# Optimization experiments

Measured on AMD Instinct MI355X. Metric: run time of the kernel, lower is better.

The kernel has to match this reference:

```python
import jax, jax.numpy as jnp
import numpy as np
import math

EMBED_DIM = 1024
NUM_HEADS = 16
HEAD_DIM = EMBED_DIM // NUM_HEADS


def setup_inputs() -> dict:
    key = jax.random.key(0)
    ks = jax.random.split(key, 12)
    B, N = 2, 2048
    s = 1.0 / math.sqrt(EMBED_DIM)
    inp = {
        "query": jax.random.normal(ks[0], (B, N, EMBED_DIM), jnp.float32),
        "key": jax.random.normal(ks[1], (B, N, EMBED_DIM), jnp.float32),
        "value": jax.random.normal(ks[2], (B, N, EMBED_DIM), jnp.float32),
        "Wq": jax.random.normal(ks[3], (EMBED_DIM, EMBED_DIM), jnp.float32) * s,
        "bq": jnp.zeros((EMBED_DIM,), jnp.float32),
        "Wk": jax.random.normal(ks[4], (EMBED_DIM, EMBED_DIM), jnp.float32) * s,
        "bk": jnp.zeros((EMBED_DIM,), jnp.float32),
        "Wv": jax.random.normal(ks[5], (EMBED_DIM, EMBED_DIM), jnp.float32) * s,
        "bv": jnp.zeros((EMBED_DIM,), jnp.float32),
        "Wo": jax.random.normal(ks[6], (EMBED_DIM, EMBED_DIM), jnp.float32) * s,
        "bo": jnp.zeros((EMBED_DIM,), jnp.float32),
        "gate": jnp.zeros((NUM_HEADS,), jnp.float32),
    }
    return inp


def reference(query, key, value, Wq, bq, Wk, bk, Wv, bv, Wo, bo, gate):
    B, Nq, _ = query.shape
    Nk = key.shape[1]
    H, D = NUM_HEADS, HEAD_DIM
    # projections (Linear: x @ W.T + b); split heads -> [B, H, N, D]
    q = (query @ Wq.T + bq).reshape(B, Nq, H, D).transpose(0, 2, 1, 3)
    k = (key @ Wk.T + bk).reshape(B, Nk, H, D).transpose(0, 2, 1, 3)
    v = (value @ Wv.T + bv).reshape(B, Nk, H, D).transpose(0, 2, 1, 3)
    # scaled logits with per-head sigmoid gate folded into the scale
    scale = jax.nn.sigmoid(gate) / math.sqrt(D)  # [H]
    logits = jnp.einsum("bhqd,bhkd->bhqk", q, k) * scale[None, :, None, None]
    attn = jax.nn.softmax(logits, axis=-1)
    out = jnp.einsum("bhqk,bhkd->bhqd", attn, v)
    out = out.transpose(0, 2, 1, 3).reshape(B, Nq, H * D)
    return out @ Wo.T + bo
```

## Files before the change

kernel.cpp:

```cpp
#include <hip/hip_runtime.h>
#include <hip/hip_bf16.h>
#include <cstdint>


#define DEV __device__ __forceinline__
typedef __attribute__((ext_vector_type(8))) short bf16x8;
typedef __attribute__((ext_vector_type(4))) float f32x4;
typedef unsigned short u16;

DEV void async16(const void* g, void* l) {
  __builtin_amdgcn_global_load_lds(
      (const __attribute__((address_space(1))) unsigned int*)g,
      (__attribute__((address_space(3))) unsigned int*)l, 16, 0, 0);
}

DEV u16 bf16_rne(float f) {
  unsigned int u = __builtin_bit_cast(unsigned int, f);
  u += 0x7FFFu + ((u >> 16) & 1u);
  return (u16)(u >> 16);
}

DEV u16 cvt16(float x) {
  __hip_bfloat16 h = __float2bfloat16(x);
  return __builtin_bit_cast(u16, h);
}

DEV unsigned pack2(float lo, float hi) {
  return (unsigned)cvt16(lo) | ((unsigned)cvt16(hi) << 16);
}

__global__ __launch_bounds__(256) void cast_all(
    const float* __restrict__ q, const float* __restrict__ k, const float* __restrict__ v,
    const float* __restrict__ Wq, const float* __restrict__ Wk,
    const float* __restrict__ Wv, const float* __restrict__ Wo,
    u16* __restrict__ XQ, u16* __restrict__ XK, u16* __restrict__ XV,
    u16* __restrict__ WQB, u16* __restrict__ WKB, u16* __restrict__ WVB,
    u16* __restrict__ WOB) {
  int idx = blockIdx.x * 256 + threadIdx.x;
  const float* src; u16* dst; int i;
  if      (idx <  524288) { src = q;  dst = XQ;  i = idx; }
  else if (idx < 1048576) { src = k;  dst = XK;  i = idx -  524288; }
  else if (idx < 1572864) { src = v;  dst = XV;  i = idx - 1048576; }
  else if (idx < 1703936) { src = Wq; dst = WQB; i = idx - 1572864; }
  else if (idx < 1835008) { src = Wk; dst = WKB; i = idx - 1703936; }
  else if (idx < 1966080) { src = Wv; dst = WVB; i = idx - 1835008; }
  else                    { src = Wo; dst = WOB; i = idx - 1966080; }
  const float4* p = (const float4*)src + (size_t)i * 2;
  float4 a = p[0], b = p[1];
  union { u16 us[8]; uint4 vv; } u;
  u.us[0] = bf16_rne(a.x); u.us[1] = bf16_rne(a.y);
  u.us[2] = bf16_rne(a.z); u.us[3] = bf16_rne(a.w);
  u.us[4] = bf16_rne(b.x); u.us[5] = bf16_rne(b.y);
  u.us[6] = bf16_rne(b.z); u.us[7] = bf16_rne(b.w);
  ((uint4*)dst)[i] = u.vv;
}

__global__ __launch_bounds__(256, 3) void gemm_qkv(
    const u16* __restrict__ XQ, const u16* __restrict__ XK, const u16* __restrict__ XV,
    const u16* __restrict__ Wb,
    const float* __restrict__ bq, const float* __restrict__ bkb, const float* __restrict__ bv,
    const float* __restrict__ gate,
    u16* __restrict__ QB, u16* __restrict__ KB, u16* __restrict__ VTB) {
  __shared__ __attribute__((aligned(16))) u16 As[2][128 * 32];
  __shared__ __attribute__((aligned(16))) u16 Bs[2][128 * 32];
  const int t = threadIdx.x, lane = t & 63, w = t >> 6;
  const int l15 = lane & 15, quad = lane >> 4;
  const int seg = blockIdx.x >> 8, inner = blockIdx.x & 255;
  const int bm = inner >> 3, bn = inner & 7;
  const int m0 = bm << 7, n0 = bn << 7;
  const u16* A = (seg == 0) ? XQ : (seg == 1) ? XK : XV;
  const u16* W = Wb + (long)seg * 1048576;
  const int wm = (w >> 1) << 6, wn = (w & 1) << 6;
  const int r0 = t >> 2, cc0 = (t & 3) * 8;
  const u16* gA0 = A + (long)(m0 + r0) * 1024 + cc0;
  const u16* gA1 = gA0 + 64 * 1024;
  const u16* gB0 = W + (long)(n0 + r0) * 1024 + cc0;
  const u16* gB1 = gB0 + 64 * 1024;

  async16(gA0, &As[0][t * 8]); async16(gA1, &As[0][(t + 256) * 8]);
  async16(gB0, &Bs[0][t * 8]); async16(gB1, &Bs[0][(t + 256) * 8]);

  f32x4 acc[4][4] = {};
  for (int k0 = 0; k0 < 1024; k0 += 32) {
    const int cur = (k0 >> 5) & 1;
    __syncthreads();
    if (k0 + 32 < 1024) {
      const int kn = k0 + 32, nb = cur ^ 1;
      async16(gA0 + kn, &As[nb][t * 8]); async16(gA1 + kn, &As[nb][(t + 256) * 8]);
      async16(gB0 + kn, &Bs[nb][t * 8]); async16(gB1 + kn, &Bs[nb][(t + 256) * 8]);
    }
    bf16x8 af[4], bfm[4];
#pragma unroll
    for (int i = 0; i < 4; i++)
      af[i] = *(const bf16x8*)&As[cur][(wm + i * 16 + l15) * 32 + quad * 8];
#pragma unroll
    for (int j = 0; j < 4; j++)
      bfm[j] = *(const bf16x8*)&Bs[cur][(wn + j * 16 + l15) * 32 + quad * 8];
#pragma unroll
    for (int i = 0; i < 4; i++)
#pragma unroll
      for (int j = 0; j < 4; j++)
        acc[i][j] = __builtin_amdgcn_mfma_f32_16x16x32_bf16(af[i], bfm[j], acc[i][j], 0, 0, 0);
  }

  if (seg == 2) {
#pragma unroll
    for (int i = 0; i < 4; i++) {
      int token = m0 + wm + i * 16 + quad * 4;
      int bb_ = token >> 11, n = token & 2047;
#pragma unroll
      for (int j = 0; j < 4; j++) {
        int col = n0 + wn + j * 16 + l15;
        float bb = bv[col];
        union { u16 us[4]; uint2 u2; } pk;
#pragma unroll
        for (int r = 0; r < 4; r++) pk.us[r] = bf16_rne(acc[i][j][r] + bb);
        *(uint2*)&VTB[(long)(bb_ * 1024 + col) * 2048 + n] = pk.u2;
      }
    }
  } else {
    const float* bias = seg ? bkb : bq;
    u16* C = seg ? KB : QB;
#pragma unroll
    for (int j = 0; j < 4; j++) {
      int col = n0 + wn + j * 16 + l15;
      float bb = bias[col];
      float scl = 1.f;
      if (seg == 0) {
        float g = gate[col >> 6];
        float sig = 1.f / (1.f + __builtin_amdgcn_exp2f(-g * 1.44269504f));
        scl = sig * 0.125f * 1.44269504f;
      }
#pragma unroll
      for (int i = 0; i < 4; i++) {
        int row = m0 + wm + i * 16 + quad * 4;
#pragma unroll
        for (int r = 0; r < 4; r++)
          C[(long)(row + r) * 1024 + col] = bf16_rne((acc[i][j][r] + bb) * scl);
      }
    }
  }
}

__global__ __launch_bounds__(256, 2) void gemm_out(
    const u16* __restrict__ A, const u16* __restrict__ W,
    const float* __restrict__ bias, float* __restrict__ Cf) {
  __shared__ __attribute__((aligned(16))) u16 As[2][64 * 32];
  __shared__ __attribute__((aligned(16))) u16 Bs[2][128 * 32];
  const int t = threadIdx.x, lane = t & 63, w = t >> 6;
  const int l15 = lane & 15, quad = lane >> 4;
  const int bm = blockIdx.x >> 3, bn = blockIdx.x & 7;
  const int m0 = bm << 6, n0 = bn << 7;
  const int wm = (w >> 1) << 5, wn = (w & 1) << 6;
  const int r0 = t >> 2, cc0 = (t & 3) * 8;
  const u16* gA = A + (long)(m0 + r0) * 1024 + cc0;
  const u16* gB0 = W + (long)(n0 + r0) * 1024 + cc0;
  const u16* gB1 = gB0 + 64 * 1024;

  async16(gA, &As[0][t * 8]);
  async16(gB0, &Bs[0][t * 8]); async16(gB1, &Bs[0][(t + 256) * 8]);

  f32x4 acc[2][4] = {};
  for (int k0 = 0; k0 < 1024; k0 += 32) {
    const int cur = (k0 >> 5) & 1;
    __syncthreads();
    if (k0 + 32 < 1024) {
      const int kn = k0 + 32, nb = cur ^ 1;
      async16(gA + kn, &As[nb][t * 8]);
      async16(gB0 + kn, &Bs[nb][t * 8]); async16(gB1 + kn, &Bs[nb][(t + 256) * 8]);
    }
    bf16x8 af[2], bfm[4];
#pragma unroll
    for (int i = 0; i < 2; i++)
      af[i] = *(const bf16x8*)&As[cur][(wm + i * 16 + l15) * 32 + quad * 8];
#pragma unroll
    for (int j = 0; j < 4; j++)
      bfm[j] = *(const bf16x8*)&Bs[cur][(wn + j * 16 + l15) * 32 + quad * 8];
#pragma unroll
    for (int i = 0; i < 2; i++)
#pragma unroll
      for (int j = 0; j < 4; j++)
        acc[i][j] = __builtin_amdgcn_mfma_f32_16x16x32_bf16(af[i], bfm[j], acc[i][j], 0, 0, 0);
  }

#pragma unroll
  for (int j = 0; j < 4; j++) {
    int col = n0 + wn + j * 16 + l15;
    float bb = bias[col];
#pragma unroll
    for (int i = 0; i < 2; i++) {
      int row = m0 + wm + i * 16 + quad * 4;
#pragma unroll
      for (int r = 0; r < 4; r++)
        Cf[(long)(row + r) * 1024 + col] = acc[i][j][r] + bb;
    }
  }
}

__global__ __launch_bounds__(128, 4) void attn_kernel(
    const u16* __restrict__ Q, const u16* __restrict__ Kb,
    const u16* __restrict__ Vt, u16* __restrict__ Op, float* __restrict__ lp) {
  __shared__ __attribute__((aligned(16))) u16 Ks[2][32 * 64];
  __shared__ __attribute__((aligned(16))) u16 Vs[2][64 * 32];
  __shared__ __attribute__((aligned(16))) u16 Ps[2][32 * 32];
  const int t = threadIdx.x, lane = t & 63, w = t >> 6;
  const int l15 = lane & 15, quad = lane >> 4;
  const int qt = blockIdx.x >> 1, ksp = blockIdx.x & 1;
  const int h = blockIdx.y, b = blockIdx.z;
  const int q0 = qt * 64, tok0 = b * 2048, key0 = ksp * 1024;
  const u16* Kbase = Kb + (long)tok0 * 1024 + h * 64;
  const u16* Vbase = Vt + (long)(b * 1024 + h * 64) * 2048;

  bf16x8 aq[2][2];
#pragma unroll
  for (int i = 0; i < 2; i++) {
    long row = tok0 + q0 + w * 32 + i * 16 + l15;
#pragma unroll
    for (int ks = 0; ks < 2; ks++)
      aq[i][ks] = *(const bf16x8*)&Q[row * 1024 + h * 64 + ks * 32 + quad * 8];
  }

#pragma unroll
  for (int i = 0; i < 2; i++) {
    int c = i * 128 + t;
    int rk = c >> 3, ck = c & 7, cks = ck ^ ((rk >> 1) & 7);
    async16(&Kbase[(long)(key0 + rk) * 1024 + cks * 8], &Ks[0][c * 8]);
    int rv = c >> 2, cv = c & 3, cvs = cv ^ ((rv >> 1) & 3);
    async16(&Vbase[(long)rv * 2048 + key0 + cvs * 8], &Vs[0][c * 8]);
  }

  float l_st[2][4] = {};
  f32x4 O[2][4] = {};

  for (int kt = 0; kt < 32; kt++) {
    const int cur = kt & 1;
    __syncthreads();
    if (kt + 1 < 32) {
      const int k0n = key0 + (kt + 1) * 32, nb = cur ^ 1;
#pragma unroll
      for (int i = 0; i < 2; i++) {
        int c = i * 128 + t;
        int rk = c >> 3, ck = c & 7, cks = ck ^ ((rk >> 1) & 7);
        async16(&Kbase[(long)(k0n + rk) * 1024 + cks * 8], &Ks[nb][c * 8]);
        int rv = c >> 2, cv = c & 3, cvs = cv ^ ((rv >> 1) & 3);
        async16(&Vbase[(long)rv * 2048 + k0n + cvs * 8], &Vs[nb][c * 8]);
      }
    }

    f32x4 s[2][2] = {};
#pragma unroll
    for (int ks = 0; ks < 2; ks++) {
      bf16x8 bk_[2];
#pragma unroll
      for (int j = 0; j < 2; j++) {
        int rl = 2 * l15 + j;
        bk_[j] = *(const bf16x8*)&Ks[cur][rl * 64 + (((ks * 4 + quad) ^ (l15 & 7))) * 8];
      }
#pragma unroll
      for (int i = 0; i < 2; i++)
#pragma unroll
        for (int j = 0; j < 2; j++)
          s[i][j] = __builtin_amdgcn_mfma_f32_16x16x32_bf16(aq[i][ks], bk_[j], s[i][j], 0, 0, 0);
    }

#pragma unroll
    for (int i = 0; i < 2; i++) {
#pragma unroll
      for (int r = 0; r < 4; r++) {
        float p0 = __builtin_amdgcn_exp2f(s[i][0][r]);
        float p1 = __builtin_amdgcn_exp2f(s[i][1][r]);
        l_st[i][r] += p0 + p1;
        const int prow = i * 16 + quad * 4 + r;
        const int chs = (l15 >> 2) ^ ((prow >> 1) & 3);
        *(unsigned*)&Ps[w][prow * 32 + chs * 8 + (l15 & 3) * 2] = pack2(p0, p1);
      }
    }

    {
      bf16x8 ap[2], bv_[4];
#pragma unroll
      for (int i = 0; i < 2; i++) {
        int rl = i * 16 + l15;
        ap[i] = *(const bf16x8*)&Ps[w][rl * 32 + ((quad ^ ((rl >> 1) & 3))) * 8];
      }
#pragma unroll
      for (int dj = 0; dj < 4; dj++) {
        int rl = dj * 16 + l15;
        bv_[dj] = *(const bf16x8*)&Vs[cur][rl * 32 + ((quad ^ ((rl >> 1) & 3))) * 8];
      }
#pragma unroll
      for (int i = 0; i < 2; i++)
#pragma unroll
        for (int dj = 0; dj < 4; dj++)
          O[i][dj] = __builtin_amdgcn_mfma_f32_16x16x32_bf16(ap[i], bv_[dj], O[i][dj], 0, 0, 0);
    }
  }

#pragma unroll
  for (int i = 0; i < 2; i++) {
#pragma unroll
    for (int r = 0; r < 4; r++) {
      float ls = l_st[i][r];
      ls += __shfl_xor(ls, 1); ls += __shfl_xor(ls, 2);
      ls += __shfl_xor(ls, 4); ls += __shfl_xor(ls, 8);
      long row = tok0 + q0 + w * 32 + i * 16 + quad * 4 + r;
#pragma unroll
      for (int dj = 0; dj < 4; dj++)
        Op[(long)ksp * 4194304 + row * 1024 + h * 64 + dj * 16 + l15] = cvt16(O[i][dj][r]);
      if (l15 == 0) lp[ksp * 65536 + (int)row * 16 + h] = ls;
    }
  }
}

__global__ __launch_bounds__(256) void merge_kernel(
    const u16* __restrict__ Op, const float* __restrict__ lp,
    u16* __restrict__ AO) {
  int idx = blockIdx.x * 256 + threadIdx.x;
  int tok = idx >> 7, rem = idx & 127, h = rem >> 3;
  float inv = 1.f / (lp[tok * 16 + h] + lp[65536 + tok * 16 + h]);
  union { uint4 v; u16 us[8]; } ua, ub, uo;
  ua.v = ((const uint4*)Op)[idx];
  ub.v = ((const uint4*)Op)[idx + 524288];
#pragma unroll
  for (int j = 0; j < 8; j++) {
    float fa = __builtin_bit_cast(float, (unsigned)((unsigned)ua.us[j] << 16));
    float fb = __builtin_bit_cast(float, (unsigned)((unsigned)ub.us[j] << 16));
    uo.us[j] = cvt16((fa + fb) * inv);
  }
  ((uint4*)AO)[idx] = uo.v;
}

extern "C" void kernel_launch(void* const* d_in, const int* in_sizes, int n_in,
                              void* d_out, int out_size, void* d_ws, size_t ws_size,
                              hipStream_t stream) {
  const float* q  = (const float*)d_in[0];
  const float* k  = (const float*)d_in[1];
  const float* v  = (const float*)d_in[2];
  const float* Wq = (const float*)d_in[3];
  const float* bq = (const float*)d_in[4];
  const float* Wk = (const float*)d_in[5];
  const float* bk = (const float*)d_in[6];
  const float* Wv = (const float*)d_in[7];
  const float* bv = (const float*)d_in[8];
  const float* Wo = (const float*)d_in[9];
  const float* bo = (const float*)d_in[10];
  const float* gate = (const float*)d_in[11];
  float* out = (float*)d_out;
  char* ws = (char*)d_ws;

  const size_t MB = 1u << 20;
  u16* WQB = (u16*)(ws + 0 * MB);
  u16* WKB = (u16*)(ws + 2 * MB);
  u16* WVB = (u16*)(ws + 4 * MB);
  u16* WOB = (u16*)(ws + 6 * MB);
  u16* XQ  = (u16*)(ws + 8 * MB);
  u16* XK  = (u16*)(ws + 16 * MB);
  u16* XV  = (u16*)(ws + 24 * MB);
  u16* QB  = (u16*)(ws + 32 * MB);
  u16* KB  = (u16*)(ws + 40 * MB);
  u16* AOB = (u16*)(ws + 8 * MB);
  u16* OPp = (u16*)(ws + 16 * MB);
  float* LP = (float*)(ws + 0 * MB);
  u16* VTB = (u16*)d_out;

  cast_all<<<8192, 256, 0, stream>>>(q, k, v, Wq, Wk, Wv, Wo,
                                     XQ, XK, XV, WQB, WKB, WVB, WOB);
  gemm_qkv<<<768, 256, 0, stream>>>(XQ, XK, XV, WQB, bq, bk, bv, gate, QB, KB, VTB);
  attn_kernel<<<dim3(64, 16, 2), 128, 0, stream>>>(QB, KB, VTB, OPp, LP);
  merge_kernel<<<2048, 256, 0, stream>>>(OPp, LP, AOB);
  gemm_out<<<512, 256, 0, stream>>>(AOB, WOB, bo, out);
}
```

Before: 239.9 us.

## Split attention keys four ways and read V fragments directly from global

The attention kernel now splits the key range into four 512-key chunks instead of two, doubling the grid to raise parallelism and occupancy. V tiles are no longer staged through LDS; each lane loads its bf16x8 V fragments straight from global memory. MFMA sections are wrapped in s_setprio, and the P-tile LDS row swizzle is altered. The merge kernel now combines four partials, with the fourth stored in spare output memory. This adds partial-output write/read traffic and exposes global-load latency for V in exchange for lower LDS usage and more blocks.

```diff
diff --git a/kernel.cpp b/kernel.cpp
--- a/kernel.cpp
+++ b/kernel.cpp
@@ -197,19 +197,19 @@
   }
 }
 
-__global__ __launch_bounds__(128, 4) void attn_kernel(
+__global__ __launch_bounds__(128, 5) void attn_kernel(
     const u16* __restrict__ Q, const u16* __restrict__ Kb,
-    const u16* __restrict__ Vt, u16* __restrict__ Op, float* __restrict__ lp) {
+    const u16* __restrict__ Vt, u16* __restrict__ Op0, u16* __restrict__ Op3,
+    float* __restrict__ lp) {
   __shared__ __attribute__((aligned(16))) u16 Ks[2][32 * 64];
-  __shared__ __attribute__((aligned(16))) u16 Vs[2][64 * 32];
   __shared__ __attribute__((aligned(16))) u16 Ps[2][32 * 32];
   const int t = threadIdx.x, lane = t & 63, w = t >> 6;
   const int l15 = lane & 15, quad = lane >> 4;
-  const int qt = blockIdx.x >> 1, ksp = blockIdx.x & 1;
+  const int qt = blockIdx.x >> 2, ksp = blockIdx.x & 3;
   const int h = blockIdx.y, b = blockIdx.z;
-  const int q0 = qt * 64, tok0 = b * 2048, key0 = ksp * 1024;
+  const int q0 = qt * 64, tok0 = b * 2048, key0 = ksp * 512;
   const u16* Kbase = Kb + (long)tok0 * 1024 + h * 64;
-  const u16* Vbase = Vt + (long)(b * 1024 + h * 64) * 2048;
+  const u16* Vbase = Vt + (long)(b * 1024 + h * 64) * 2048 + key0;
 
   bf16x8 aq[2][2];
 #pragma unroll
@@ -225,29 +225,26 @@
     int c = i * 128 + t;
     int rk = c >> 3, ck = c & 7, cks = ck ^ ((rk >> 1) & 7);
     async16(&Kbase[(long)(key0 + rk) * 1024 + cks * 8], &Ks[0][c * 8]);
-    int rv = c >> 2, cv = c & 3, cvs = cv ^ ((rv >> 1) & 3);
-    async16(&Vbase[(long)rv * 2048 + key0 + cvs * 8], &Vs[0][c * 8]);
   }
 
   float l_st[2][4] = {};
   f32x4 O[2][4] = {};
 
-  for (int kt = 0; kt < 32; kt++) {
+  for (int kt = 0; kt < 16; kt++) {
     const int cur = kt & 1;
     __syncthreads();
-    if (kt + 1 < 32) {
+    if (kt + 1 < 16) {
       const int k0n = key0 + (kt + 1) * 32, nb = cur ^ 1;
 #pragma unroll
       for (int i = 0; i < 2; i++) {
         int c = i * 128 + t;
         int rk = c >> 3, ck = c & 7, cks = ck ^ ((rk >> 1) & 7);
         async16(&Kbase[(long)(k0n + rk) * 1024 + cks * 8], &Ks[nb][c * 8]);
-        int rv = c >> 2, cv = c & 3, cvs = cv ^ ((rv >> 1) & 3);
-        async16(&Vbase[(long)rv * 2048 + k0n + cvs * 8], &Vs[nb][c * 8]);
       }
     }
 
     f32x4 s[2][2] = {};
+    __builtin_amdgcn_s_setprio(1);
 #pragma unroll
     for (int ks = 0; ks < 2; ks++) {
       bf16x8 bk_[2];
@@ -262,6 +259,7 @@
         for (int j = 0; j < 2; j++)
           s[i][j] = __builtin_amdgcn_mfma_f32_16x16x32_bf16(aq[i][ks], bk_[j], s[i][j], 0, 0, 0);
     }
+    __builtin_amdgcn_s_setprio(0);
 
 #pragma unroll
     for (int i = 0; i < 2; i++) {
@@ -271,31 +269,36 @@
         float p1 = __builtin_amdgcn_exp2f(s[i][1][r]);
         l_st[i][r] += p0 + p1;
         const int prow = i * 16 + quad * 4 + r;
+        const int pr = prow ^ ((prow >> 2) & 1);
         const int chs = (l15 >> 2) ^ ((prow >> 1) & 3);
-        *(unsigned*)&Ps[w][prow * 32 + chs * 8 + (l15 & 3) * 2] = pack2(p0, p1);
-      }
-    }
+        *(unsigned*)&Ps[w][pr * 32 + chs * 8 + (l15 & 3) * 2] = pack2(p0, p1);
+      }
+    }
+
+    bf16x8 bv_[4];
+#pragma unroll
+    for (int dj = 0; dj < 4; dj++)
+      bv_[dj] = *(const bf16x8*)&Vbase[(long)(dj * 16 + l15) * 2048 + kt * 32 + quad * 8];
 
     {
-      bf16x8 ap[2], bv_[4];
+      bf16x8 ap[2];
 #pragma unroll
       for (int i = 0; i < 2; i++) {
         int rl = i * 16 + l15;
-        ap[i] = *(const bf16x8*)&Ps[w][rl * 32 + ((quad ^ ((rl >> 1) & 3))) * 8];
-      }
-#pragma unroll
-      for (int dj = 0; dj < 4; dj++) {
-        int rl = dj * 16 + l15;
-        bv_[dj] = *(const bf16x8*)&Vs[cur][rl * 32 + ((quad ^ ((rl >> 1) & 3))) * 8];
-      }
+        int rp = rl ^ ((rl >> 2) & 1);
+        ap[i] = *(const bf16x8*)&Ps[w][rp * 32 + ((quad ^ ((rl >> 1) & 3))) * 8];
+      }
+      __builtin_amdgcn_s_setprio(1);
 #pragma unroll
       for (int i = 0; i < 2; i++)
 #pragma unroll
         for (int dj = 0; dj < 4; dj++)
           O[i][dj] = __builtin_amdgcn_mfma_f32_16x16x32_bf16(ap[i], bv_[dj], O[i][dj], 0, 0, 0);
-    }
-  }
-
+      __builtin_amdgcn_s_setprio(0);
+    }
+  }
+
+  u16* dst = (ksp == 3) ? Op3 : (Op0 + (long)ksp * 4194304);
 #pragma unroll
   for (int i = 0; i < 2; i++) {
 #pragma unroll
@@ -306,26 +309,32 @@
       long row = tok0 + q0 + w * 32 + i * 16 + quad * 4 + r;
 #pragma unroll
       for (int dj = 0; dj < 4; dj++)
-        Op[(long)ksp * 4194304 + row * 1024 + h * 64 + dj * 16 + l15] = cvt16(O[i][dj][r]);
+        dst[row * 1024 + h * 64 + dj * 16 + l15] = cvt16(O[i][dj][r]);
       if (l15 == 0) lp[ksp * 65536 + (int)row * 16 + h] = ls;
     }
   }
 }
 
 __global__ __launch_bounds__(256) void merge_kernel(
-    const u16* __restrict__ Op, const float* __restrict__ lp,
-    u16* __restrict__ AO) {
+    const u16* __restrict__ Op0, const u16* __restrict__ Op3,
+    const float* __restrict__ lp, u16* __restrict__ AO) {
   int idx = blockIdx.x * 256 + threadIdx.x;
   int tok = idx >> 7, rem = idx & 127, h = rem >> 3;
-  float inv = 1.f / (lp[tok * 16 + h] + lp[65536 + tok * 16 + h]);
-  union { uint4 v; u16 us[8]; } ua, ub, uo;
-  ua.v = ((const uint4*)Op)[idx];
-  ub.v = ((const uint4*)Op)[idx + 524288];
+  int li = tok * 16 + h;
+  float inv = 1.f / (lp[li] + lp[65536 + li] + lp[131072 + li] + lp[196608 + li]);
+  union U { uint4 v; u16 us[8]; };
+  U a0, a1, a2, a3, uo;
+  a0.v = ((const uint4*)Op0)[idx];
+  a1.v = ((const uint4*)Op0)[idx + 524288];
+  a2.v = ((const uint4*)Op0)[idx + 1048576];
+  a3.v = ((const uint4*)Op3)[idx];
 #pragma unroll
   for (int j = 0; j < 8; j++) {
-    float fa = __builtin_bit_cast(float, (unsigned)((unsigned)ua.us[j] << 16));
-    float fb = __builtin_bit_cast(float, (unsigned)((unsigned)ub.us[j] << 16));
-    uo.us[j] = cvt16((fa + fb) * inv);
+    float f0 = __builtin_bit_cast(float, (unsigned)((unsigned)a0.us[j] << 16));
+    float f1 = __builtin_bit_cast(float, (unsigned)((unsigned)a1.us[j] << 16));
+    float f2 = __builtin_bit_cast(float, (unsigned)((unsigned)a2.us[j] << 16));
+    float f3 = __builtin_bit_cast(float, (unsigned)((unsigned)a3.us[j] << 16));
+    uo.us[j] = cvt16((f0 + f1 + f2 + f3) * inv);
   }
   ((uint4*)AO)[idx] = uo.v;
 }
@@ -358,15 +367,16 @@
   u16* XV  = (u16*)(ws + 24 * MB);
   u16* QB  = (u16*)(ws + 32 * MB);
   u16* KB  = (u16*)(ws + 40 * MB);
+  u16* OPp  = (u16*)(ws + 8 * MB);
+  u16* OPd3 = (u16*)((char*)d_out + 8 * MB);
+  float* LP = (float*)(ws + 0 * MB);
   u16* AOB = (u16*)(ws + 8 * MB);
-  u16* OPp = (u16*)(ws + 16 * MB);
-  float* LP = (float*)(ws + 0 * MB);
   u16* VTB = (u16*)d_out;
 
   cast_all<<<8192, 256, 0, stream>>>(q, k, v, Wq, Wk, Wv, Wo,
                                      XQ, XK, XV, WQB, WKB, WVB, WOB);
   gemm_qkv<<<768, 256, 0, stream>>>(XQ, XK, XV, WQB, bq, bk, bv, gate, QB, KB, VTB);
-  attn_kernel<<<dim3(64, 16, 2), 128, 0, stream>>>(QB, KB, VTB, OPp, LP);
-  merge_kernel<<<2048, 256, 0, stream>>>(OPp, LP, AOB);
+  attn_kernel<<<dim3(128, 16, 2), 128, 0, stream>>>(QB, KB, VTB, OPp, OPd3, LP);
+  merge_kernel<<<2048, 256, 0, stream>>>(OPp, OPd3, LP, AOB);
   gemm_out<<<512, 256, 0, stream>>>(AOB, WOB, bo, out);
 }
```

Result: slower. 287.5 us (+19.8%).

## Keep P in registers by transposing QK MFMA, drop P shared-memory round trip

Applied to the files above, without the earlier changes.

Swaps the MFMA operand order for the QK^T product so the score tile comes out transposed, letting each lane's exp2 results pack directly into the A-operand fragment for the PV MFMA. This removes the per-wave P shared-memory buffer along with its writes and reads. The row-sum reduction moves to cross-quad shuffles. Freeing that LDS also allows raising the occupancy hint to 5 blocks, and s_setprio is added around the MFMA groups. The risk is higher register pressure under the tighter launch bound.

```diff
diff --git a/kernel.cpp b/kernel.cpp
--- a/kernel.cpp
+++ b/kernel.cpp
@@ -197,12 +197,11 @@
   }
 }
 
-__global__ __launch_bounds__(128, 4) void attn_kernel(
+__global__ __launch_bounds__(128, 5) void attn_kernel(
     const u16* __restrict__ Q, const u16* __restrict__ Kb,
     const u16* __restrict__ Vt, u16* __restrict__ Op, float* __restrict__ lp) {
   __shared__ __attribute__((aligned(16))) u16 Ks[2][32 * 64];
   __shared__ __attribute__((aligned(16))) u16 Vs[2][64 * 32];
-  __shared__ __attribute__((aligned(16))) u16 Ps[2][32 * 32];
   const int t = threadIdx.x, lane = t & 63, w = t >> 6;
   const int l15 = lane & 15, quad = lane >> 4;
   const int qt = blockIdx.x >> 1, ksp = blockIdx.x & 1;
@@ -229,7 +228,7 @@
     async16(&Vbase[(long)rv * 2048 + key0 + cvs * 8], &Vs[0][c * 8]);
   }
 
-  float l_st[2][4] = {};
+  float l_st[2] = {};
   f32x4 O[2][4] = {};
 
   for (int kt = 0; kt < 32; kt++) {
@@ -248,6 +247,7 @@
     }
 
     f32x4 s[2][2] = {};
+    __builtin_amdgcn_s_setprio(1);
 #pragma unroll
     for (int ks = 0; ks < 2; ks++) {
       bf16x8 bk_[2];
@@ -260,54 +260,53 @@
       for (int i = 0; i < 2; i++)
 #pragma unroll
         for (int j = 0; j < 2; j++)
-          s[i][j] = __builtin_amdgcn_mfma_f32_16x16x32_bf16(aq[i][ks], bk_[j], s[i][j], 0, 0, 0);
-    }
-
+          s[i][j] = __builtin_amdgcn_mfma_f32_16x16x32_bf16(bk_[j], aq[i][ks], s[i][j], 0, 0, 0);
+    }
+    __builtin_amdgcn_s_setprio(0);
+
+    bf16x8 ap[2];
 #pragma unroll
     for (int i = 0; i < 2; i++) {
+      union { unsigned uw[4]; bf16x8 v8; } pw;
 #pragma unroll
       for (int r = 0; r < 4; r++) {
         float p0 = __builtin_amdgcn_exp2f(s[i][0][r]);
         float p1 = __builtin_amdgcn_exp2f(s[i][1][r]);
-        l_st[i][r] += p0 + p1;
-        const int prow = i * 16 + quad * 4 + r;
-        const int chs = (l15 >> 2) ^ ((prow >> 1) & 3);
-        *(unsigned*)&Ps[w][prow * 32 + chs * 8 + (l15 & 3) * 2] = pack2(p0, p1);
-      }
-    }
-
-    {
-      bf16x8 ap[2], bv_[4];
-#pragma unroll
-      for (int i = 0; i < 2; i++) {
-        int rl = i * 16 + l15;
-        ap[i] = *(const bf16x8*)&Ps[w][rl * 32 + ((quad ^ ((rl >> 1) & 3))) * 8];
-      }
-#pragma unroll
-      for (int dj = 0; dj < 4; dj++) {
-        int rl = dj * 16 + l15;
-        bv_[dj] = *(const bf16x8*)&Vs[cur][rl * 32 + ((quad ^ ((rl >> 1) & 3))) * 8];
-      }
-#pragma unroll
-      for (int i = 0; i < 2; i++)
-#pragma unroll
-        for (int dj = 0; dj < 4; dj++)
-          O[i][dj] = __builtin_amdgcn_mfma_f32_16x16x32_bf16(ap[i], bv_[dj], O[i][dj], 0, 0, 0);
-    }
+        l_st[i] += p0 + p1;
+        pw.uw[r] = pack2(p0, p1);
+      }
+      ap[i] = pw.v8;
+    }
+
+    bf16x8 bv_[4];
+#pragma unroll
+    for (int dj = 0; dj < 4; dj++) {
+      int rl = dj * 16 + l15;
+      bv_[dj] = *(const bf16x8*)&Vs[cur][rl * 32 + ((quad ^ ((rl >> 1) & 3))) * 8];
+    }
+    __builtin_amdgcn_s_setprio(1);
+#pragma unroll
+    for (int i = 0; i < 2; i++)
+#pragma unroll
+      for (int dj = 0; dj < 4; dj++)
+        O[i][dj] = __builtin_amdgcn_mfma_f32_16x16x32_bf16(ap[i], bv_[dj], O[i][dj], 0, 0, 0);
+    __builtin_amdgcn_s_setprio(0);
   }
 
 #pragma unroll
   for (int i = 0; i < 2; i++) {
+    float ls = l_st[i];
+    ls += __shfl_xor(ls, 16); ls += __shfl_xor(ls, 32);
+    if (quad == 0) {
+      long qrow = tok0 + q0 + w * 32 + i * 16 + l15;
+      lp[ksp * 65536 + (int)qrow * 16 + h] = ls;
+    }
 #pragma unroll
     for (int r = 0; r < 4; r++) {
-      float ls = l_st[i][r];
-      ls += __shfl_xor(ls, 1); ls += __shfl_xor(ls, 2);
-      ls += __shfl_xor(ls, 4); ls += __shfl_xor(ls, 8);
       long row = tok0 + q0 + w * 32 + i * 16 + quad * 4 + r;
 #pragma unroll
       for (int dj = 0; dj < 4; dj++)
         Op[(long)ksp * 4194304 + row * 1024 + h * 64 + dj * 16 + l15] = cvt16(O[i][dj][r]);
-      if (l15 == 0) lp[ksp * 65536 + (int)row * 16 + h] = ls;
     }
   }
 }
```

Result: no change. 238.8 us (-0.5%).
